# Performance work log

Measured on AMD Instinct MI355X. Metric: run time of the kernel, lower is better.

Reference implementation:

```python
import jax, jax.numpy as jnp
import numpy as np

EPS = 1e-6
QMAX = 127.0  # hif8 emulated as symmetric 8-bit fake-quant (true hif8 numerics are proprietary)


def _rotate_half(v):
    d = v.shape[-1] // 2
    return jnp.concatenate([-v[..., d:], v[..., :d]], axis=-1)


def _quant(v):
    # per-row (last-axis) absmax quantization emulating hif8 with a per-tensor-row scale
    amax = jnp.max(jnp.abs(v), axis=-1, keepdims=True)
    scale = jnp.maximum(amax / QMAX, 1e-8)
    q = jnp.round(v / scale)
    return q, jnp.squeeze(scale, -1)


def setup_inputs() -> dict:
    key = jax.random.key(0)
    ks = jax.random.split(key, 16)
    B, S, H, Hn, D, L = 2, 4096, 2048, 32, 128, 16384
    return {
        "x": jax.random.normal(ks[0], (B, S, H), jnp.float32),
        "q_norm": jax.random.uniform(ks[1], (H,), jnp.float32),
        "q_norm_scale": jax.random.uniform(ks[2], (H,), jnp.float32),
        "w_qb": jax.random.normal(ks[3], (H, Hn * D), jnp.float32),
        "w_qb_scale": jax.random.uniform(ks[4], (Hn * D,), jnp.float32),
        "wk": jax.random.normal(ks[5], (H, D), jnp.float32),
        "w_proj": jax.random.normal(ks[6], (H, Hn), jnp.float32),
        "ln_gamma_k": jax.random.uniform(ks[7], (H,), jnp.float32),
        "ln_beta_k": jax.random.normal(ks[8], (H,), jnp.float32),
        "cos_idx_rope": jax.random.uniform(ks[9], (S, D), jnp.float32),
        "sin_idx_rope": jax.random.uniform(ks[10], (S, D), jnp.float32),
        "hadamard_q": jax.random.normal(ks[11], (D, D), jnp.float32),
        "hadamard_k": jax.random.normal(ks[12], (D, D), jnp.float32),
        "k_cache": jnp.zeros((L, D), jnp.float32),
        "k_cache_scale": jnp.zeros((L,), jnp.float32),
        "k_cache_index": jnp.arange(B * S, dtype=jnp.int32).reshape(B, S),
    }


def reference(x, q_norm, q_norm_scale, w_qb, w_qb_scale, wk, w_proj,
              ln_gamma_k, ln_beta_k, cos_idx_rope, sin_idx_rope,
              hadamard_q, hadamard_k, k_cache, k_cache_scale, k_cache_index):
    B, S, H = x.shape
    D = hadamard_q.shape[0]
    Hn = w_qb.shape[1] // D

    # ---- Q branch: RMSNorm + smooth scale -> quantized GEMM (dequant fused) ----
    rms = jax.lax.rsqrt(jnp.mean(x * x, axis=-1, keepdims=True) + EPS)
    xq = x * rms * q_norm * q_norm_scale                      # [B,S,H]
    q = jnp.einsum('bsh,hd->bsd', xq, w_qb) * w_qb_scale      # [B,S,Hn*D]
    q = q.reshape(B, S, Hn, D)

    cos_q = cos_idx_rope[:S][None, :, None, :]
    sin_q = sin_idx_rope[:S][None, :, None, :]
    q = q * cos_q + _rotate_half(q) * sin_q                   # RoPE
    q = jnp.einsum('bshd,de->bshe', q, hadamard_q)            # Hadamard mix
    q_hif8, q_scale = _quant(q)                               # [B,S,Hn,D], [B,S,Hn]

    # ---- K branch: LayerNorm -> proj -> RoPE -> Hadamard -> quant ----
    mu = jnp.mean(x, axis=-1, keepdims=True)
    var = jnp.mean(jnp.square(x - mu), axis=-1, keepdims=True)
    xk = (x - mu) * jax.lax.rsqrt(var + EPS) * ln_gamma_k + ln_beta_k
    k = jnp.einsum('bsh,hd->bsd', xk, wk)                     # [B,S,D]
    cos_k = cos_idx_rope[:S][None, :, :]
    sin_k = sin_idx_rope[:S][None, :, :]
    k = k * cos_k + _rotate_half(k) * sin_k
    k = jnp.einsum('bsd,de->bse', k, hadamard_k)
    k_q, k_s = _quant(k)                                      # [B,S,D], [B,S]

    # ---- scatter quantized K into the indexer cache ----
    idx = k_cache_index.reshape(-1)
    k_hif8 = k_cache.at[idx].set(k_q.reshape(-1, D))
    k_scale = k_cache_scale.at[idx].set(k_s.reshape(-1))

    # ---- per-head indexer weights ----
    weights = jnp.einsum('bsh,he->bse', x, w_proj)            # [B,S,Hn]

    return (q_hif8, q_scale, k_hif8, k_scale, weights)
```

## Files before the change

### kernel.cpp

```cpp
#include <hip/hip_runtime.h>
#include <hip/hip_bf16.h>
#include <stdint.h>

constexpr int Mrows = 8192;
constexpr int Hdim  = 2048;
constexpr int Sdim  = 4096;
constexpr int HnD   = 4096;
constexpr int Hn    = 32;
constexpr int Dd    = 128;
constexpr int Lc    = 16384;
constexpr int NFULL = 4352;

typedef unsigned short u16;
typedef __attribute__((ext_vector_type(8))) short    bf16x8;
typedef __attribute__((ext_vector_type(4))) float    f32x4;
typedef __attribute__((ext_vector_type(8))) unsigned short u16x8;

__device__ __forceinline__ float bf2f(u16 u) {
    union { unsigned int i; float f; } v; v.i = ((unsigned int)u) << 16; return v.f;
}
__device__ __forceinline__ u16 f2bf(float f) {
    union { float f; unsigned int i; } v; v.f = f;
    unsigned int x = v.i;
    return (u16)((x + 0x7fffu + ((x >> 16) & 1u)) >> 16);
}
__device__ __forceinline__ void gload_lds16(const void* g, void* l) {
    __builtin_amdgcn_global_load_lds(
        (const __attribute__((address_space(1))) void*)g,
        (__attribute__((address_space(3))) void*)l, 16, 0, 0);
}

__global__ __launch_bounds__(256) void stats_cvt(
    const float* __restrict__ x, u16* __restrict__ xb, float* __restrict__ rms,
    float* __restrict__ mu, float* __restrict__ rstd)
{
    int r = blockIdx.x, t = threadIdx.x;
    const float4* xr = (const float4*)(x + (size_t)r * Hdim);
    float4 a = xr[2 * t], bq = xr[2 * t + 1];
    float v[8] = {a.x, a.y, a.z, a.w, bq.x, bq.y, bq.z, bq.w};
    float s = 0.f, ss = 0.f;
    __align__(16) u16 o[8];
    #pragma unroll
    for (int i = 0; i < 8; i++) { s += v[i]; ss += v[i] * v[i]; o[i] = f2bf(v[i]); }
    ((u16x8*)(xb + (size_t)r * Hdim))[t] = *(const u16x8*)o;
    for (int oo = 32; oo > 0; oo >>= 1) { s += __shfl_down(s, oo); ss += __shfl_down(ss, oo); }
    __shared__ float as[4], ass[4];
    if ((t & 63) == 0) { as[t >> 6] = s; ass[t >> 6] = ss; }
    __syncthreads();
    if (t == 0) {
        float S1 = as[0] + as[1] + as[2] + as[3];
        float S2 = ass[0] + ass[1] + ass[2] + ass[3];
        float mean = S1 / Hdim, msq = S2 / Hdim;
        rms[r]  = rsqrtf(msq + 1e-6f);
        mu[r]   = mean;
        rstd[r] = rsqrtf(msq - mean * mean + 1e-6f);
    }
}

__global__ __launch_bounds__(256) void prep_wt(
    const float* __restrict__ wqb, const float* __restrict__ qn, const float* __restrict__ qns,
    const float* __restrict__ wk,  const float* __restrict__ g,  const float* __restrict__ wproj,
    u16* __restrict__ wt)
{
    __shared__ u16 tile[64][72];
    int k0 = blockIdx.x * 64, n0 = blockIdx.y * 64;
    int t = threadIdx.x;
    int lk = t >> 2, lc0 = (t & 3) * 16;
    int k = k0 + lk;
    float c1k = qn[k] * qns[k];
    float gk  = g[k];
    #pragma unroll
    for (int i = 0; i < 16; i++) {
        int n = n0 + lc0 + i;
        float val;
        if (n < 4096)      val = wqb[(size_t)k * HnD + n] * c1k;
        else if (n < 4224) val = wk[k * Dd + (n - 4096)] * gk;
        else if (n < 4256) val = wproj[k * Hn + (n - 4224)];
        else               val = 0.f;
        tile[lk][lc0 + i] = f2bf(val);
    }
    __syncthreads();
    int ln = t >> 2, lk0 = (t & 3) * 16;
    __align__(16) u16 o[16];
    #pragma unroll
    for (int i = 0; i < 16; i++) o[i] = tile[lk0 + i][ln];
    u16* dst = wt + (size_t)(n0 + ln) * Hdim + k0 + lk0;
    *(u16x8*)dst = *(const u16x8*)o;
    *(u16x8*)(dst + 8) = *((const u16x8*)o + 1);
}

__global__ __launch_bounds__(256) void transpose_h(
    const float* __restrict__ hq, const float* __restrict__ hk,
    u16* __restrict__ hqt, u16* __restrict__ hkt)
{
    __shared__ float tile[128][129];
    const float* src = blockIdx.x ? hk : hq;
    u16* dst = blockIdx.x ? hkt : hqt;
    int t = threadIdx.x;
    int r = t >> 1, h = (t & 1) * 64;
    #pragma unroll
    for (int j = 0; j < 16; j++) {
        float4 v = *(const float4*)(src + r * Dd + h + 4 * j);
        tile[r][h + 4 * j]     = v.x;
        tile[r][h + 4 * j + 1] = v.y;
        tile[r][h + 4 * j + 2] = v.z;
        tile[r][h + 4 * j + 3] = v.w;
    }
    __syncthreads();
    #pragma unroll
    for (int j0 = 0; j0 < 64; j0 += 8) {
        __align__(16) u16 o[8];
        #pragma unroll
        for (int j = 0; j < 8; j++) o[j] = f2bf(tile[h + j0 + j][r]);
        *(u16x8*)(dst + r * Dd + h + j0) = *(const u16x8*)o;
    }
}

__global__ __launch_bounds__(256) void bg_dot(
    const float* __restrict__ wk, const float* __restrict__ g, const float* __restrict__ b,
    float* __restrict__ bdot, float* __restrict__ gdot)
{
    int n = blockIdx.x, t = threadIdx.x;
    float sb = 0.f, sg = 0.f;
    for (int k = t; k < Hdim; k += 256) {
        float w = wk[k * Dd + n];
        sb += b[k] * w;
        sg += g[k] * w;
    }
    for (int o = 32; o > 0; o >>= 1) { sb += __shfl_down(sb, o); sg += __shfl_down(sg, o); }
    __shared__ float rb[4], rg[4];
    if ((t & 63) == 0) { rb[t >> 6] = sb; rg[t >> 6] = sg; }
    __syncthreads();
    if (t == 0) { bdot[n] = rb[0] + rb[1] + rb[2] + rb[3]; gdot[n] = rg[0] + rg[1] + rg[2] + rg[3]; }
}

#define LDA_(buf, kk, mt) (*(const bf16x8*)(lds + (buf)*65536 + (kk)*16384 + \
    (wr*64 + (mt)*16 + l15) * 64 + qsw))
#define LDB_(buf, kk, nt) (*(const bf16x8*)(lds + (buf)*65536 + 32768 + (kk)*16384 + \
    (wc*128 + (nt)*16 + l15) * 64 + qsw))
#define STG_A(bufb, kk, rh, kt) gload_lds16( \
    Ab + (size_t)((rh)*128 + lrow) * Hdim + (kt)*64 + (kk)*32 + gcol, \
    lds + (bufb)*65536 + (kk)*16384 + (rh)*8192 + wq1024)
#define STG_B(bufb, kk, rh, kt) gload_lds16( \
    Bb + (size_t)((rh)*128 + lrow) * Hdim + (kt)*64 + (kk)*32 + gcol, \
    lds + (bufb)*65536 + 32768 + (kk)*16384 + (rh)*8192 + wq1024)
#define MFMA16(AV, NB) do { \
    _Pragma("unroll") \
    for (int mt = 0; mt < 4; mt++) \
        _Pragma("unroll") \
        for (int nt = 0; nt < 4; nt++) \
            acc[mt][(NB)*4 + nt] = __builtin_amdgcn_mfma_f32_16x16x32_bf16( \
                AV[mt], bfr[nt], acc[mt][(NB)*4 + nt], 0, 0, 0); \
} while (0)

__global__ __launch_bounds__(512, 2) void main_gemm(
    const u16* __restrict__ A, const u16* __restrict__ Bt,
    const float* __restrict__ rms, const float* __restrict__ mu, const float* __restrict__ rstd,
    const float* __restrict__ qbs,
    const float* __restrict__ bdot, const float* __restrict__ gdot,
    const u16* __restrict__ hqt,
    const float* __restrict__ cosr, const float* __restrict__ sinr,
    float* __restrict__ oq, float* __restrict__ oqs,
    float* __restrict__ kpre, float* __restrict__ wout)
{
    __shared__ __align__(16) char lds[131072];

    int tid = threadIdx.x;
    int w = tid >> 6, lane = tid & 63, quad = lane >> 4, l15 = lane & 15;
    int wr = w >> 1, wc = w & 1;
    int bm = blockIdx.x, bn = blockIdx.y;
    int brow = bm * 256;
    int qsw = (quad ^ ((l15 >> 1) & 3)) * 16;

    const u16* Ab = A  + (size_t)brow * Hdim;
    const u16* Bb = Bt + (size_t)(bn * 256) * Hdim;

    int lrow = tid >> 2;
    int gcol = (((tid & 3) ^ ((lrow >> 1) & 3)) * 8);
    int wq1024 = w * 1024;

    f32x4 acc[4][8] = {};

    STG_A(0, 0, 0, 0); STG_A(0, 0, 1, 0); STG_B(0, 0, 0, 0); STG_B(0, 0, 1, 0);
    STG_A(0, 1, 0, 0); STG_A(0, 1, 1, 0); STG_B(0, 1, 0, 0); STG_B(0, 1, 1, 0);
    asm volatile("s_waitcnt vmcnt(4)" ::: "memory");
    __builtin_amdgcn_sched_barrier(0);
    __builtin_amdgcn_s_barrier();

    for (int t = 0; t < 32; t++) {
        int buf = t & 1, nb = buf ^ 1;
        bool pf = (t < 31);
        bf16x8 a0[4], bfr[4];
        #pragma unroll
        for (int mt = 0; mt < 4; mt++) a0[mt] = LDA_(buf, 0, mt);
        #pragma unroll
        for (int nt = 0; nt < 4; nt++) bfr[nt] = LDB_(buf, 0, nt);
        if (pf) { STG_A(nb, 0, 0, t+1); STG_A(nb, 0, 1, t+1); STG_B(nb, 0, 0, t+1); STG_B(nb, 0, 1, t+1); }
        asm volatile("s_waitcnt lgkmcnt(0)" ::: "memory");
        __builtin_amdgcn_sched_barrier(0);
        __builtin_amdgcn_s_setprio(1);
        MFMA16(a0, 0);
        __builtin_amdgcn_s_setprio(0);
        __builtin_amdgcn_s_barrier();
        #pragma unroll
        for (int nt = 0; nt < 4; nt++) bfr[nt] = LDB_(buf, 0, 4 + nt);
        if (pf) { STG_A(nb, 1, 0, t+1); STG_A(nb, 1, 1, t+1); STG_B(nb, 1, 0, t+1); STG_B(nb, 1, 1, t+1); }
        asm volatile("s_waitcnt lgkmcnt(0)" ::: "memory");
        __builtin_amdgcn_sched_barrier(0);
        __builtin_amdgcn_s_setprio(1);
        MFMA16(a0, 1);
        __builtin_amdgcn_s_setprio(0);
        if (pf) { asm volatile("s_waitcnt vmcnt(8)" ::: "memory"); }
        else    { asm volatile("s_waitcnt vmcnt(0)" ::: "memory"); }
        __builtin_amdgcn_sched_barrier(0);
        __builtin_amdgcn_s_barrier();
        #pragma unroll
        for (int mt = 0; mt < 4; mt++) a0[mt] = LDA_(buf, 1, mt);
        #pragma unroll
        for (int nt = 0; nt < 4; nt++) bfr[nt] = LDB_(buf, 1, nt);
        asm volatile("s_waitcnt lgkmcnt(0)" ::: "memory");
        __builtin_amdgcn_sched_barrier(0);
        __builtin_amdgcn_s_setprio(1);
        MFMA16(a0, 0);
        __builtin_amdgcn_s_setprio(0);
        __builtin_amdgcn_s_barrier();
        #pragma unroll
        for (int nt = 0; nt < 4; nt++) bfr[nt] = LDB_(buf, 1, 4 + nt);
        asm volatile("s_waitcnt lgkmcnt(0)" ::: "memory");
        __builtin_amdgcn_sched_barrier(0);
        __builtin_amdgcn_s_setprio(1);
        MFMA16(a0, 1);
        __builtin_amdgcn_s_setprio(0);
        asm volatile("s_waitcnt vmcnt(4)" ::: "memory");
        __builtin_amdgcn_sched_barrier(0);
        __builtin_amdgcn_s_barrier();
    }

    if (bn < 16) {
        __syncthreads();
        int head = bn * 2 + wc;
        char* Pw = lds + w * 16384;
        float qb[8];
        #pragma unroll
        for (int nt = 0; nt < 8; nt++) qb[nt] = qbs[head * 128 + nt * 16 + l15];
        #pragma unroll
        for (int mt = 0; mt < 4; mt++) {
            float y[8][4];
            #pragma unroll
            for (int reg = 0; reg < 4; reg++) {
                float rv = rms[brow + wr * 64 + mt * 16 + quad * 4 + reg];
                #pragma unroll
                for (int nt = 0; nt < 8; nt++) y[nt][reg] = acc[mt][nt][reg] * rv * qb[nt];
            }
            #pragma unroll
            for (int reg = 0; reg < 4; reg++) {
                int rp = mt * 16 + quad * 4 + reg;
                int s_ = (brow + wr * 64 + rp) & (Sdim - 1);
                const float* cr = cosr + (size_t)s_ * Dd + l15;
                const float* sr = sinr + (size_t)s_ * Dd + l15;
                int sw = (rp & 7) << 4;
                #pragma unroll
                for (int nt = 0; nt < 8; nt++) {
                    float c  = cr[nt * 16];
                    float sv = sr[nt * 16];
                    float sign = (nt < 4) ? -1.f : 1.f;
                    float o = y[nt][reg] * c + sign * y[nt ^ 4][reg] * sv;
                    int colb = (nt * 16 + l15) * 2;
                    *(u16*)(Pw + rp * 256 + (colb ^ sw)) = f2bf(o);
                }
            }
        }
        __syncthreads();
        #pragma unroll
        for (int mt = 0; mt < 4; mt++) {
            bf16x8 pa[4];
            #pragma unroll
            for (int kb = 0; kb < 4; kb++) {
                int row = mt * 16 + l15;
                pa[kb] = *(const bf16x8*)(Pw + row * 256 + ((kb * 64 + quad * 16) ^ ((row & 7) << 4)));
            }
            f32x4 a2[8] = {};
            #pragma unroll
            for (int nt = 0; nt < 8; nt++) {
                #pragma unroll
                for (int kb = 0; kb < 4; kb++) {
                    bf16x8 hb = *(const bf16x8*)(hqt + (size_t)(nt * 16 + l15) * Dd + kb * 32 + quad * 8);
                    a2[nt] = __builtin_amdgcn_mfma_f32_16x16x32_bf16(pa[kb], hb, a2[nt], 0, 0, 0);
                }
            }
            #pragma unroll
            for (int reg = 0; reg < 4; reg++) {
                float m = 0.f;
                #pragma unroll
                for (int nt = 0; nt < 8; nt++) m = fmaxf(m, fabsf(a2[nt][reg]));
                m = fmaxf(m, __shfl_xor(m, 8));
                m = fmaxf(m, __shfl_xor(m, 4));
                m = fmaxf(m, __shfl_xor(m, 2));
                m = fmaxf(m, __shfl_xor(m, 1));
                float scale = fmaxf(m * (1.f / 127.f), 1e-8f);
                float inv = 1.f / scale;
                int r = brow + wr * 64 + mt * 16 + quad * 4 + reg;
                float* orow = oq + (size_t)r * HnD + head * 128;
                #pragma unroll
                for (int nt = 0; nt < 8; nt++)
                    orow[nt * 16 + l15] = rintf(a2[nt][reg] * inv);
                if (l15 == 0) oqs[(size_t)r * Hn + head] = scale;
            }
        }
    } else {
        if (wc == 0) {
            float bd[8], gd[8];
            #pragma unroll
            for (int nt = 0; nt < 8; nt++) { bd[nt] = bdot[nt * 16 + l15]; gd[nt] = gdot[nt * 16 + l15]; }
            #pragma unroll
            for (int mt = 0; mt < 4; mt++)
                #pragma unroll
                for (int reg = 0; reg < 4; reg++) {
                    int r = brow + wr * 64 + mt * 16 + quad * 4 + reg;
                    float sd = rstd[r], m_ = mu[r];
                    #pragma unroll
                    for (int nt = 0; nt < 8; nt++)
                        kpre[(size_t)r * Dd + nt * 16 + l15] = acc[mt][nt][reg] * sd + bd[nt] - sd * m_ * gd[nt];
                }
        } else {
            #pragma unroll
            for (int mt = 0; mt < 4; mt++)
                #pragma unroll
                for (int reg = 0; reg < 4; reg++) {
                    int r = brow + wr * 64 + mt * 16 + quad * 4 + reg;
                    #pragma unroll
                    for (int nt = 0; nt < 2; nt++)
                        wout[(size_t)r * Hn + nt * 16 + l15] = acc[mt][nt][reg];
                }
        }
    }
}

__global__ void copy_cache(const float* __restrict__ kc, const float* __restrict__ kcs,
                           float* __restrict__ dk, float* __restrict__ dks)
{
    int g = blockIdx.x * 256 + threadIdx.x;
    ((float4*)dk)[2 * g]     = ((const float4*)kc)[2 * g];
    ((float4*)dk)[2 * g + 1] = ((const float4*)kc)[2 * g + 1];
    if (g < Lc / 8) {
        ((float4*)dks)[2 * g]     = ((const float4*)kcs)[2 * g];
        ((float4*)dks)[2 * g + 1] = ((const float4*)kcs)[2 * g + 1];
    }
}

template <int IS_K>
__global__ __launch_bounds__(256) void post_kernel(
    const float* src,
    const u16* __restrict__ ht,
    const float* __restrict__ cosr, const float* __restrict__ sinr,
    const int* __restrict__ idx,
    float* dstq, float* __restrict__ dsts)
{
    constexpr int RP = 136;
    __shared__ __align__(16) u16 sA[32 * RP];
    __shared__ __align__(16) u16 sB[128 * RP];
    __shared__ float pamax[32][2];
    __shared__ int sidx[32];

    int blk = blockIdx.x, tid = threadIdx.x;

    {
        int n = tid >> 1, kk0 = (tid & 1) * 64;
        const u16x8* gp = (const u16x8*)(ht + n * Dd + kk0);
        u16* lb = sB + n * RP + kk0;
        #pragma unroll
        for (int j = 0; j < 8; j++) *(u16x8*)(lb + j * 8) = gp[j];
    }
    {
        int r = tid >> 3, c = tid & 7;
        int d0 = c * 16;
        int s_ = IS_K ? ((blk * 32 + r) & (Sdim - 1)) : (blk & (Sdim - 1));
        const float* srow = src + (size_t)blk * 4096 + r * Dd;
        int p0 = (d0 + 64) & 127;
        float sign = (d0 < 64) ? -1.f : 1.f;
        float vv[16], pv[16], cv[16], sv[16];
        #pragma unroll
        for (int j = 0; j < 4; j++) {
            float4 a = *(const float4*)(srow + d0 + 4 * j);
            float4 p = *(const float4*)(srow + p0 + 4 * j);
            float4 cc = *(const float4*)(cosr + (size_t)s_ * Dd + d0 + 4 * j);
            float4 sc = *(const float4*)(sinr + (size_t)s_ * Dd + d0 + 4 * j);
            vv[4*j] = a.x; vv[4*j+1] = a.y; vv[4*j+2] = a.z; vv[4*j+3] = a.w;
            pv[4*j] = p.x; pv[4*j+1] = p.y; pv[4*j+2] = p.z; pv[4*j+3] = p.w;
            cv[4*j] = cc.x; cv[4*j+1] = cc.y; cv[4*j+2] = cc.z; cv[4*j+3] = cc.w;
            sv[4*j] = sc.x; sv[4*j+1] = sc.y; sv[4*j+2] = sc.z; sv[4*j+3] = sc.w;
        }
        __align__(16) u16 o[16];
        #pragma unroll
        for (int i = 0; i < 16; i++)
            o[i] = f2bf(vv[i] * cv[i] + sign * pv[i] * sv[i]);
        u16* la = sA + r * RP + d0;
        *(u16x8*)la = *(const u16x8*)o;
        *(u16x8*)(la + 8) = *((const u16x8*)o + 1);
        if (IS_K && tid < 32) sidx[tid] = idx[blk * 32 + tid];
    }
    __syncthreads();

    int w = tid >> 6, lane = tid & 63, quad = lane >> 4, l15 = lane & 15;
    int rs = (w & 1) * 16, cg = (w >> 1) * 64;
    f32x4 acc[4] = {};
    #pragma unroll
    for (int kb = 0; kb < 4; kb++) {
        bf16x8 a = *(const bf16x8*)(sA + (rs + l15) * RP + kb * 32 + quad * 8);
        #pragma unroll
        for (int nt = 0; nt < 4; nt++) {
            bf16x8 b = *(const bf16x8*)(sB + (cg + nt * 16 + l15) * RP + kb * 32 + quad * 8);
            acc[nt] = __builtin_amdgcn_mfma_f32_16x16x32_bf16(a, b, acc[nt], 0, 0, 0);
        }
    }
    #pragma unroll
    for (int reg = 0; reg < 4; reg++) {
        float m = 0.f;
        #pragma unroll
        for (int nt = 0; nt < 4; nt++) m = fmaxf(m, fabsf(acc[nt][reg]));
        m = fmaxf(m, __shfl_xor(m, 8));
        m = fmaxf(m, __shfl_xor(m, 4));
        m = fmaxf(m, __shfl_xor(m, 2));
        m = fmaxf(m, __shfl_xor(m, 1));
        if (l15 == 0) pamax[rs + quad * 4 + reg][w >> 1] = m;
    }
    __syncthreads();
    #pragma unroll
    for (int reg = 0; reg < 4; reg++) {
        int r = rs + quad * 4 + reg;
        float am = fmaxf(pamax[r][0], pamax[r][1]);
        float scale = fmaxf(am * (1.f / 127.f), 1e-8f);
        float inv = 1.f / scale;
        size_t dro = IS_K ? (size_t)sidx[r] * Dd : (size_t)blk * 4096 + (size_t)r * Dd;
        #pragma unroll
        for (int nt = 0; nt < 4; nt++)
            dstq[dro + cg + nt * 16 + l15] = rintf(acc[nt][reg] * inv);
        if (l15 == 0 && (w >> 1) == 0)
            dsts[IS_K ? sidx[r] : blk * Hn + r] = scale;
    }
}

extern "C" void kernel_launch(void* const* d_in, const int* in_sizes, int n_in,
                              void* d_out, int out_size, void* d_ws, size_t ws_size,
                              hipStream_t stream) {
    (void)in_sizes; (void)n_in; (void)out_size; (void)ws_size;
    const float* x    = (const float*)d_in[0];
    const float* qn   = (const float*)d_in[1];
    const float* qns  = (const float*)d_in[2];
    const float* wqb  = (const float*)d_in[3];
    const float* wqbs = (const float*)d_in[4];
    const float* wk   = (const float*)d_in[5];
    const float* wpj  = (const float*)d_in[6];
    const float* g    = (const float*)d_in[7];
    const float* b    = (const float*)d_in[8];
    const float* cosr = (const float*)d_in[9];
    const float* sinr = (const float*)d_in[10];
    const float* hq   = (const float*)d_in[11];
    const float* hk   = (const float*)d_in[12];
    const float* kc   = (const float*)d_in[13];
    const float* kcs  = (const float*)d_in[14];
    const int*   idx  = (const int*)d_in[15];

    char* ws = (char*)d_ws;
    size_t o = 0;
    u16* xb  = (u16*)(ws + o); o += (size_t)Mrows * Hdim * 2;
    u16* wt  = (u16*)(ws + o); o += (size_t)NFULL * Hdim * 2;
    u16* hqt = (u16*)(ws + o); o += Dd * Dd * 2;
    u16* hkt = (u16*)(ws + o); o += Dd * Dd * 2;
    float* rmsb  = (float*)(ws + o); o += (size_t)Mrows * 4;
    float* mub   = (float*)(ws + o); o += (size_t)Mrows * 4;
    float* rstdb = (float*)(ws + o); o += (size_t)Mrows * 4;
    float* bdotb = (float*)(ws + o); o += 512;
    float* gdotb = (float*)(ws + o); o += 512;
    float* kpre  = (float*)(ws + o); o += (size_t)Mrows * Dd * 4;

    float* out = (float*)d_out;
    float* oq  = out;
    float* oqs = oq  + (size_t)Mrows * HnD;
    float* ok  = oqs + (size_t)Mrows * Hn;
    float* oks = ok  + (size_t)Lc * Dd;
    float* ow  = oks + Lc;

    stats_cvt<<<Mrows, 256, 0, stream>>>(x, xb, rmsb, mub, rstdb);
    prep_wt<<<dim3(Hdim / 64, NFULL / 64), 256, 0, stream>>>(wqb, qn, qns, wk, g, wpj, wt);
    transpose_h<<<2, 256, 0, stream>>>(hq, hk, hqt, hkt);
    bg_dot<<<Dd, 256, 0, stream>>>(wk, g, b, bdotb, gdotb);
    main_gemm<<<dim3(32, 17), 512, 0, stream>>>(
        xb, wt, rmsb, mub, rstdb, wqbs, bdotb, gdotb, hqt, cosr, sinr, oq, oqs, kpre, ow);
    copy_cache<<<(Lc * Dd / 8) / 256, 256, 0, stream>>>(kc, kcs, ok, oks);
    post_kernel<1><<<Mrows / 32, 256, 0, stream>>>(kpre, hkt, cosr, sinr, idx, ok, oks);
}
```

Baseline: 508.3 us.

## Split K/weights GEMM into separate kernel and retile Q GEMM with triple-buffered pipeline

```diff
diff --git a/kernel.cpp b/kernel.cpp
--- a/kernel.cpp
+++ b/kernel.cpp
@@ -134,206 +134,212 @@
     if (t == 0) { bdot[n] = rb[0] + rb[1] + rb[2] + rb[3]; gdot[n] = rg[0] + rg[1] + rg[2] + rg[3]; }
 }
 
-#define LDA_(buf, kk, mt) (*(const bf16x8*)(lds + (buf)*65536 + (kk)*16384 + \
+#define QLDA(slotb, mt) (*(const bf16x8*)(lds + (slotb) + \
     (wr*64 + (mt)*16 + l15) * 64 + qsw))
-#define LDB_(buf, kk, nt) (*(const bf16x8*)(lds + (buf)*65536 + 32768 + (kk)*16384 + \
+#define QLDB(slotb, nt) (*(const bf16x8*)(lds + (slotb) + 8192 + \
     (wc*128 + (nt)*16 + l15) * 64 + qsw))
-#define STG_A(bufb, kk, rh, kt) gload_lds16( \
-    Ab + (size_t)((rh)*128 + lrow) * Hdim + (kt)*64 + (kk)*32 + gcol, \
-    lds + (bufb)*65536 + (kk)*16384 + (rh)*8192 + wq1024)
-#define STG_B(bufb, kk, rh, kt) gload_lds16( \
-    Bb + (size_t)((rh)*128 + lrow) * Hdim + (kt)*64 + (kk)*32 + gcol, \
-    lds + (bufb)*65536 + 32768 + (kk)*16384 + (rh)*8192 + wq1024)
-#define MFMA16(AV, NB) do { \
-    _Pragma("unroll") \
-    for (int mt = 0; mt < 4; mt++) \
-        _Pragma("unroll") \
-        for (int nt = 0; nt < 4; nt++) \
-            acc[mt][(NB)*4 + nt] = __builtin_amdgcn_mfma_f32_16x16x32_bf16( \
-                AV[mt], bfr[nt], acc[mt][(NB)*4 + nt], 0, 0, 0); \
+#define QSTG(slotb, sidx) do { \
+    gload_lds16(Ab + (size_t)(arow)       * Hdim + (sidx) * 32 + acol, lds + (slotb) + wq); \
+    gload_lds16(Ab + (size_t)(64 + arow)  * Hdim + (sidx) * 32 + acol, lds + (slotb) + 4096 + wq); \
+    gload_lds16(Bb + (size_t)(arow)       * Hdim + (sidx) * 32 + acol, lds + (slotb) + 8192 + wq); \
+    gload_lds16(Bb + (size_t)(64 + arow)  * Hdim + (sidx) * 32 + acol, lds + (slotb) + 12288 + wq); \
+    gload_lds16(Bb + (size_t)(128 + arow) * Hdim + (sidx) * 32 + acol, lds + (slotb) + 16384 + wq); \
+    gload_lds16(Bb + (size_t)(192 + arow) * Hdim + (sidx) * 32 + acol, lds + (slotb) + 20480 + wq); \
 } while (0)
 
-__global__ __launch_bounds__(512, 2) void main_gemm(
+__global__ __launch_bounds__(256, 2) void main_gemm(
     const u16* __restrict__ A, const u16* __restrict__ Bt,
-    const float* __restrict__ rms, const float* __restrict__ mu, const float* __restrict__ rstd,
-    const float* __restrict__ qbs,
-    const float* __restrict__ bdot, const float* __restrict__ gdot,
+    const float* __restrict__ rms, const float* __restrict__ qbs,
     const u16* __restrict__ hqt,
     const float* __restrict__ cosr, const float* __restrict__ sinr,
-    float* __restrict__ oq, float* __restrict__ oqs,
-    float* __restrict__ kpre, float* __restrict__ wout)
-{
-    __shared__ __align__(16) char lds[131072];
+    float* __restrict__ oq, float* __restrict__ oqs)
+{
+    __shared__ __align__(16) char lds[73728];
 
     int tid = threadIdx.x;
     int w = tid >> 6, lane = tid & 63, quad = lane >> 4, l15 = lane & 15;
     int wr = w >> 1, wc = w & 1;
     int bm = blockIdx.x, bn = blockIdx.y;
-    int brow = bm * 256;
+    int brow = bm * 128;
     int qsw = (quad ^ ((l15 >> 1) & 3)) * 16;
 
     const u16* Ab = A  + (size_t)brow * Hdim;
     const u16* Bb = Bt + (size_t)(bn * 256) * Hdim;
 
-    int lrow = tid >> 2;
-    int gcol = (((tid & 3) ^ ((lrow >> 1) & 3)) * 8);
-    int wq1024 = w * 1024;
+    int arow = tid >> 2;
+    int acol = (((tid & 3) ^ ((tid >> 3) & 3)) * 8);
+    int wq   = w * 1024;
 
     f32x4 acc[4][8] = {};
 
-    STG_A(0, 0, 0, 0); STG_A(0, 0, 1, 0); STG_B(0, 0, 0, 0); STG_B(0, 0, 1, 0);
-    STG_A(0, 1, 0, 0); STG_A(0, 1, 1, 0); STG_B(0, 1, 0, 0); STG_B(0, 1, 1, 0);
-    asm volatile("s_waitcnt vmcnt(4)" ::: "memory");
+    QSTG(0, 0);
+    QSTG(24576, 1);
+    asm volatile("s_waitcnt vmcnt(6)" ::: "memory");
     __builtin_amdgcn_sched_barrier(0);
     __builtin_amdgcn_s_barrier();
 
-    for (int t = 0; t < 32; t++) {
-        int buf = t & 1, nb = buf ^ 1;
-        bool pf = (t < 31);
-        bf16x8 a0[4], bfr[4];
-        #pragma unroll
-        for (int mt = 0; mt < 4; mt++) a0[mt] = LDA_(buf, 0, mt);
-        #pragma unroll
-        for (int nt = 0; nt < 4; nt++) bfr[nt] = LDB_(buf, 0, nt);
-        if (pf) { STG_A(nb, 0, 0, t+1); STG_A(nb, 0, 1, t+1); STG_B(nb, 0, 0, t+1); STG_B(nb, 0, 1, t+1); }
+    int slotb = 0;
+    for (int s = 0; s < 64; s++) {
+        bf16x8 af[4], bq[8];
+        #pragma unroll
+        for (int mt = 0; mt < 4; mt++) af[mt] = QLDA(slotb, mt);
+        #pragma unroll
+        for (int nt = 0; nt < 8; nt++) bq[nt] = QLDB(slotb, nt);
+        if (s + 2 < 64) {
+            int ns = slotb + 49152; if (ns >= 73728) ns -= 73728;
+            QSTG(ns, s + 2);
+        }
         asm volatile("s_waitcnt lgkmcnt(0)" ::: "memory");
         __builtin_amdgcn_sched_barrier(0);
         __builtin_amdgcn_s_setprio(1);
-        MFMA16(a0, 0);
+        #pragma unroll
+        for (int mt = 0; mt < 4; mt++)
+            #pragma unroll
+            for (int nt = 0; nt < 8; nt++)
+                acc[mt][nt] = __builtin_amdgcn_mfma_f32_16x16x32_bf16(af[mt], bq[nt], acc[mt][nt], 0, 0, 0);
         __builtin_amdgcn_s_setprio(0);
-        __builtin_amdgcn_s_barrier();
-        #pragma unroll
-        for (int nt = 0; nt < 4; nt++) bfr[nt] = LDB_(buf, 0, 4 + nt);
-        if (pf) { STG_A(nb, 1, 0, t+1); STG_A(nb, 1, 1, t+1); STG_B(nb, 1, 0, t+1); STG_B(nb, 1, 1, t+1); }
-        asm volatile("s_waitcnt lgkmcnt(0)" ::: "memory");
-        __builtin_amdgcn_sched_barrier(0);
-        __builtin_amdgcn_s_setprio(1);
-        MFMA16(a0, 1);
-        __builtin_amdgcn_s_setprio(0);
-        if (pf) { asm volatile("s_waitcnt vmcnt(8)" ::: "memory"); }
-        else    { asm volatile("s_waitcnt vmcnt(0)" ::: "memory"); }
+        if (s < 62) { asm volatile("s_waitcnt vmcnt(6)" ::: "memory"); }
+        else        { asm volatile("s_waitcnt vmcnt(0)" ::: "memory"); }
         __builtin_amdgcn_sched_barrier(0);
         __builtin_amdgcn_s_barrier();
-        #pragma unroll
-        for (int mt = 0; mt < 4; mt++) a0[mt] = LDA_(buf, 1, mt);
-        #pragma unroll
-        for (int nt = 0; nt < 4; nt++) bfr[nt] = LDB_(buf, 1, nt);
-        asm volatile("s_waitcnt lgkmcnt(0)" ::: "memory");
-        __builtin_amdgcn_sched_barrier(0);
-        __builtin_amdgcn_s_setprio(1);
-        MFMA16(a0, 0);
-        __builtin_amdgcn_s_setprio(0);
-        __builtin_amdgcn_s_barrier();
-        #pragma unroll
-        for (int nt = 0; nt < 4; nt++) bfr[nt] = LDB_(buf, 1, 4 + nt);
-        asm volatile("s_waitcnt lgkmcnt(0)" ::: "memory");
-        __builtin_amdgcn_sched_barrier(0);
-        __builtin_amdgcn_s_setprio(1);
-        MFMA16(a0, 1);
-        __builtin_amdgcn_s_setprio(0);
-        asm volatile("s_waitcnt vmcnt(4)" ::: "memory");
-        __builtin_amdgcn_sched_barrier(0);
-        __builtin_amdgcn_s_barrier();
-    }
-
-    if (bn < 16) {
+        slotb += 24576; if (slotb >= 73728) slotb -= 73728;
+    }
+
+    __syncthreads();
+    int head = bn * 2 + wc;
+    char* Pw = lds + w * 16384;
+    float qb[8];
+    #pragma unroll
+    for (int nt = 0; nt < 8; nt++) qb[nt] = qbs[head * 128 + nt * 16 + l15];
+    #pragma unroll
+    for (int mt = 0; mt < 4; mt++) {
+        float y[8][4];
+        #pragma unroll
+        for (int reg = 0; reg < 4; reg++) {
+            float rv = rms[brow + wr * 64 + mt * 16 + quad * 4 + reg];
+            #pragma unroll
+            for (int nt = 0; nt < 8; nt++) y[nt][reg] = acc[mt][nt][reg] * rv * qb[nt];
+        }
+        #pragma unroll
+        for (int reg = 0; reg < 4; reg++) {
+            int rp = mt * 16 + quad * 4 + reg;
+            int s_ = (brow + wr * 64 + rp) & (Sdim - 1);
+            const float* cr = cosr + (size_t)s_ * Dd + l15;
+            const float* sr = sinr + (size_t)s_ * Dd + l15;
+            int sw = (rp & 7) << 4;
+            #pragma unroll
+            for (int nt = 0; nt < 8; nt++) {
+                float c  = cr[nt * 16];
+                float sv = sr[nt * 16];
+                float sign = (nt < 4) ? -1.f : 1.f;
+                float o = y[nt][reg] * c + sign * y[nt ^ 4][reg] * sv;
+                int colb = (nt * 16 + l15) * 2;
+                *(u16*)(Pw + rp * 256 + (colb ^ sw)) = f2bf(o);
+            }
+        }
+    }
+    __syncthreads();
+    #pragma unroll
+    for (int mt = 0; mt < 4; mt++) {
+        bf16x8 pa[4];
+        #pragma unroll
+        for (int kb = 0; kb < 4; kb++) {
+            int row = mt * 16 + l15;
+            pa[kb] = *(const bf16x8*)(Pw + row * 256 + ((kb * 64 + quad * 16) ^ ((row & 7) << 4)));
+        }
+        f32x4 a2[8] = {};
+        #pragma unroll
+        for (int nt = 0; nt < 8; nt++) {
+            #pragma unroll
+            for (int kb = 0; kb < 4; kb++) {
+                bf16x8 hb = *(const bf16x8*)(hqt + (size_t)(nt * 16 + l15) * Dd + kb * 32 + quad * 8);
+                a2[nt] = __builtin_amdgcn_mfma_f32_16x16x32_bf16(pa[kb], hb, a2[nt], 0, 0, 0);
+            }
+        }
+        #pragma unroll
+        for (int reg = 0; reg < 4; reg++) {
+            float m = 0.f;
+            #pragma unroll
+            for (int nt = 0; nt < 8; nt++) m = fmaxf(m, fabsf(a2[nt][reg]));
+            m = fmaxf(m, __shfl_xor(m, 8));
+            m = fmaxf(m, __shfl_xor(m, 4));
+            m = fmaxf(m, __shfl_xor(m, 2));
+            m = fmaxf(m, __shfl_xor(m, 1));
+            float scale = fmaxf(m * (1.f / 127.f), 1e-8f);
+            float inv = 1.f / scale;
+            int r = brow + wr * 64 + mt * 16 + quad * 4 + reg;
+            float* orow = oq + (size_t)r * HnD + head * 128;
+            #pragma unroll
+            for (int nt = 0; nt < 8; nt++)
+                orow[nt * 16 + l15] = rintf(a2[nt][reg] * inv);
+            if (l15 == 0) oqs[(size_t)r * Hn + head] = scale;
+        }
+    }
+}
+
+__global__ __launch_bounds__(256) void kw_gemm(
+    const u16* __restrict__ A, const u16* __restrict__ Bt,
+    const float* __restrict__ rstd, const float* __restrict__ mu,
+    const float* __restrict__ bdot, const float* __restrict__ gdot,
+    float* __restrict__ kpre, float* __restrict__ wout)
+{
+    __shared__ __align__(16) u16 sA[32 * 64];
+    __shared__ __align__(16) u16 sB[192 * 64];
+    int tid = threadIdx.x, w = tid >> 6, lane = tid & 63, quad = lane >> 4, l15 = lane & 15;
+    int blk = blockIdx.x;
+    const u16* Ab = A  + (size_t)(blk * 32) * Hdim;
+    const u16* Bb = Bt + (size_t)4096 * Hdim;
+
+    f32x4 acc[2][3] = {};
+
+    for (int s = 0; s < 32; s++) {
         __syncthreads();
-        int head = bn * 2 + wc;
-        char* Pw = lds + w * 16384;
-        float qb[8];
-        #pragma unroll
-        for (int nt = 0; nt < 8; nt++) qb[nt] = qbs[head * 128 + nt * 16 + l15];
-        #pragma unroll
-        for (int mt = 0; mt < 4; mt++) {
-            float y[8][4];
-            #pragma unroll
-            for (int reg = 0; reg < 4; reg++) {
-                float rv = rms[brow + wr * 64 + mt * 16 + quad * 4 + reg];
+        {
+            int row = tid >> 3, ch = (tid & 7) ^ (row & 7);
+            gload_lds16(Ab + (size_t)row * Hdim + s * 64 + ch * 8, (char*)sA + w * 1024);
+        }
+        #pragma unroll
+        for (int u = 0; u < 6; u++) {
+            int idx = u * 256 + tid;
+            int row = idx >> 3, ch = (idx & 7) ^ (row & 7);
+            gload_lds16(Bb + (size_t)row * Hdim + s * 64 + ch * 8,
+                        (char*)sB + u * 4096 + w * 1024);
+        }
+        __syncthreads();
+        #pragma unroll
+        for (int kk = 0; kk < 2; kk++) {
+            bf16x8 af[2], bf[3];
+            #pragma unroll
+            for (int m = 0; m < 2; m++) {
+                int row = m * 16 + l15;
+                af[m] = *(const bf16x8*)(sA + row * 64 + (((kk * 4 + quad) ^ (row & 7)) * 8));
+            }
+            #pragma unroll
+            for (int j = 0; j < 3; j++) {
+                int row = (w * 3 + j) * 16 + l15;
+                bf[j] = *(const bf16x8*)(sB + row * 64 + (((kk * 4 + quad) ^ (row & 7)) * 8));
+            }
+            #pragma unroll
+            for (int m = 0; m < 2; m++)
                 #pragma unroll
-                for (int nt = 0; nt < 8; nt++) y[nt][reg] = acc[mt][nt][reg] * rv * qb[nt];
+                for (int j = 0; j < 3; j++)
+                    acc[m][j] = __builtin_amdgcn_mfma_f32_16x16x32_bf16(af[m], bf[j], acc[m][j], 0, 0, 0);
+        }
+    }
+    #pragma unroll
+    for (int m = 0; m < 2; m++)
+        #pragma unroll
+        for (int reg = 0; reg < 4; reg++) {
+            int r = blk * 32 + m * 16 + quad * 4 + reg;
+            float sd = rstd[r], m_ = mu[r];
+            #pragma unroll
+            for (int j = 0; j < 3; j++) {
+                int f = w * 3 + j, c = f * 16 + l15;
+                float v = acc[m][j][reg];
+                if (f < 8)       kpre[(size_t)r * Dd + c] = v * sd + bdot[c] - sd * m_ * gdot[c];
+                else if (f < 10) wout[(size_t)r * Hn + (c - 128)] = v;
             }
-            #pragma unroll
-            for (int reg = 0; reg < 4; reg++) {
-                int rp = mt * 16 + quad * 4 + reg;
-                int s_ = (brow + wr * 64 + rp) & (Sdim - 1);
-                const float* cr = cosr + (size_t)s_ * Dd + l15;
-                const float* sr = sinr + (size_t)s_ * Dd + l15;
-                int sw = (rp & 7) << 4;
-                #pragma unroll
-                for (int nt = 0; nt < 8; nt++) {
-                    float c  = cr[nt * 16];
-                    float sv = sr[nt * 16];
-                    float sign = (nt < 4) ? -1.f : 1.f;
-                    float o = y[nt][reg] * c + sign * y[nt ^ 4][reg] * sv;
-                    int colb = (nt * 16 + l15) * 2;
-                    *(u16*)(Pw + rp * 256 + (colb ^ sw)) = f2bf(o);
-                }
-            }
-        }
-        __syncthreads();
-        #pragma unroll
-        for (int mt = 0; mt < 4; mt++) {
-            bf16x8 pa[4];
-            #pragma unroll
-            for (int kb = 0; kb < 4; kb++) {
-                int row = mt * 16 + l15;
-                pa[kb] = *(const bf16x8*)(Pw + row * 256 + ((kb * 64 + quad * 16) ^ ((row & 7) << 4)));
-            }
-            f32x4 a2[8] = {};
-            #pragma unroll
-            for (int nt = 0; nt < 8; nt++) {
-                #pragma unroll
-                for (int kb = 0; kb < 4; kb++) {
-                    bf16x8 hb = *(const bf16x8*)(hqt + (size_t)(nt * 16 + l15) * Dd + kb * 32 + quad * 8);
-                    a2[nt] = __builtin_amdgcn_mfma_f32_16x16x32_bf16(pa[kb], hb, a2[nt], 0, 0, 0);
-                }
-            }
-            #pragma unroll
-            for (int reg = 0; reg < 4; reg++) {
-                float m = 0.f;
-                #pragma unroll
-                for (int nt = 0; nt < 8; nt++) m = fmaxf(m, fabsf(a2[nt][reg]));
-                m = fmaxf(m, __shfl_xor(m, 8));
-                m = fmaxf(m, __shfl_xor(m, 4));
-                m = fmaxf(m, __shfl_xor(m, 2));
-                m = fmaxf(m, __shfl_xor(m, 1));
-                float scale = fmaxf(m * (1.f / 127.f), 1e-8f);
-                float inv = 1.f / scale;
-                int r = brow + wr * 64 + mt * 16 + quad * 4 + reg;
-                float* orow = oq + (size_t)r * HnD + head * 128;
-                #pragma unroll
-                for (int nt = 0; nt < 8; nt++)
-                    orow[nt * 16 + l15] = rintf(a2[nt][reg] * inv);
-                if (l15 == 0) oqs[(size_t)r * Hn + head] = scale;
-            }
-        }
-    } else {
-        if (wc == 0) {
-            float bd[8], gd[8];
-            #pragma unroll
-            for (int nt = 0; nt < 8; nt++) { bd[nt] = bdot[nt * 16 + l15]; gd[nt] = gdot[nt * 16 + l15]; }
-            #pragma unroll
-            for (int mt = 0; mt < 4; mt++)
-                #pragma unroll
-                for (int reg = 0; reg < 4; reg++) {
-                    int r = brow + wr * 64 + mt * 16 + quad * 4 + reg;
-                    float sd = rstd[r], m_ = mu[r];
-                    #pragma unroll
-                    for (int nt = 0; nt < 8; nt++)
-                        kpre[(size_t)r * Dd + nt * 16 + l15] = acc[mt][nt][reg] * sd + bd[nt] - sd * m_ * gd[nt];
-                }
-        } else {
-            #pragma unroll
-            for (int mt = 0; mt < 4; mt++)
-                #pragma unroll
-                for (int reg = 0; reg < 4; reg++) {
-                    int r = brow + wr * 64 + mt * 16 + quad * 4 + reg;
-                    #pragma unroll
-                    for (int nt = 0; nt < 2; nt++)
-                        wout[(size_t)r * Hn + nt * 16 + l15] = acc[mt][nt][reg];
-                }
-        }
-    }
+        }
 }
 
 __global__ void copy_cache(const float* __restrict__ kc, const float* __restrict__ kcs,
@@ -485,8 +491,9 @@
     prep_wt<<<dim3(Hdim / 64, NFULL / 64), 256, 0, stream>>>(wqb, qn, qns, wk, g, wpj, wt);
     transpose_h<<<2, 256, 0, stream>>>(hq, hk, hqt, hkt);
     bg_dot<<<Dd, 256, 0, stream>>>(wk, g, b, bdotb, gdotb);
-    main_gemm<<<dim3(32, 17), 512, 0, stream>>>(
-        xb, wt, rmsb, mub, rstdb, wqbs, bdotb, gdotb, hqt, cosr, sinr, oq, oqs, kpre, ow);
+    kw_gemm<<<Mrows / 32, 256, 0, stream>>>(xb, wt, rstdb, mub, bdotb, gdotb, kpre, ow);
+    main_gemm<<<dim3(Mrows / 128, 16), 256, 0, stream>>>(
+        xb, wt, rmsb, wqbs, hqt, cosr, sinr, oq, oqs);
     copy_cache<<<(Lc * Dd / 8) / 256, 256, 0, stream>>>(kc, kcs, ok, oks);
     post_kernel<1><<<Mrows / 32, 256, 0, stream>>>(kpre, hkt, cosr, sinr, idx, ok, oks);
 }
```

Result: faster. 496.9 us (-2.2%).
